# Kernel optimization log

Hardware: AMD Instinct MI355X
Metric: run time of the kernel (lower is better)

The kernel has to match this reference:

```python
import jax, jax.numpy as jnp
import numpy as np

D_MODEL = 1024
N_HEADS = 16
D_K = D_MODEL // N_HEADS
LN_EPS = 1e-5
NEG = -1e9


def setup_inputs() -> dict:
    key = jax.random.key(0)
    ks = jax.random.split(key, 12)
    B, S = 4, 2048
    s = 1.0 / np.sqrt(D_MODEL)
    # causal mask (1 = keep, 0 = masked)
    causal = jnp.tril(jnp.ones((S, S), dtype=jnp.int32))
    mask = jnp.broadcast_to(causal[None, None], (B, 1, S, S))
    return {
        "Q": jax.random.normal(ks[0], (B, S, D_MODEL), jnp.float32),
        "K": jax.random.normal(ks[1], (B, S, D_MODEL), jnp.float32),
        "V": jax.random.normal(ks[2], (B, S, D_MODEL), jnp.float32),
        "mask": mask,
        "Wq": jax.random.normal(ks[3], (D_MODEL, D_MODEL), jnp.float32) * s,
        "bq": jnp.zeros((D_MODEL,), jnp.float32),
        "Wk": jax.random.normal(ks[4], (D_MODEL, D_MODEL), jnp.float32) * s,
        "bk": jnp.zeros((D_MODEL,), jnp.float32),
        "Wv": jax.random.normal(ks[5], (D_MODEL, D_MODEL), jnp.float32) * s,
        "bv": jnp.zeros((D_MODEL,), jnp.float32),
        "Wo": jax.random.normal(ks[6], (D_MODEL, D_MODEL), jnp.float32) * s,
        "bo": jnp.zeros((D_MODEL,), jnp.float32),
        "ln_gamma": jnp.ones((D_MODEL,), jnp.float32),
        "ln_beta": jnp.zeros((D_MODEL,), jnp.float32),
    }


def _split_heads(x, B, S):
    # (B,S,D) -> (B,H,S,d_k)
    return x.reshape(B, S, N_HEADS, D_K).transpose(0, 2, 1, 3)


def reference(Q, K, V, mask, Wq, bq, Wk, bk, Wv, bv, Wo, bo, ln_gamma, ln_beta):
    B, S, _ = Q.shape
    residual = Q
    q = _split_heads(Q @ Wq + bq, B, S)
    k = _split_heads(K @ Wk + bk, B, S)
    v = _split_heads(V @ Wv + bv, B, S)
    scores = jnp.einsum("bhqd,bhkd->bhqk", q, k) / np.sqrt(D_K).astype(np.float32)
    scores = jnp.where(mask == 0, jnp.float32(NEG), scores)
    attn = jax.nn.softmax(scores, axis=-1)  # dropout p=0 -> identity
    ctx = jnp.einsum("bhqk,bhkd->bhqd", attn, v)
    ctx = ctx.transpose(0, 2, 1, 3).reshape(B, S, D_MODEL)
    out = ctx @ Wo + bo
    x = out + residual
    mu = jnp.mean(x, axis=-1, keepdims=True)
    var = jnp.mean(jnp.square(x - mu), axis=-1, keepdims=True)
    y = (x - mu) * jax.lax.rsqrt(var + LN_EPS) * ln_gamma + ln_beta
    return (y, attn)
```

## Files before the change

### kernel.cpp

```cpp
#include <hip/hip_runtime.h>

#define D_MODEL 1024
#define NH 16
#define DKH 64
#define SEQ 2048
#define BATCH 4
#define ROWS (BATCH*SEQ)

typedef _Float16 f16;
typedef _Float16 f16x4 __attribute__((ext_vector_type(4)));
typedef _Float16 f16x8 __attribute__((ext_vector_type(8)));
typedef float f32x4 __attribute__((ext_vector_type(4)));

#define MFMA16(a,b,c) __builtin_amdgcn_mfma_f32_16x16x32_f16((a),(b),(c),0,0,0)

__device__ __forceinline__ void gload16(const void* g, void* l) {
  __builtin_amdgcn_global_load_lds((const __attribute__((address_space(1))) void*)g,
                                   (__attribute__((address_space(3))) void*)l,
                                   16, 0, 0);
}


__global__ __launch_bounds__(256) void cvt_w_kernel(const float* __restrict__ Wq,
    const float* __restrict__ Wk, const float* __restrict__ Wv, const float* __restrict__ Wo,
    f16* __restrict__ dst)
{
  const float* W = (blockIdx.z==0)?Wq:(blockIdx.z==1)?Wk:(blockIdx.z==2)?Wv:Wo;
  f16* d = dst + (size_t)blockIdx.z * ((size_t)D_MODEL*D_MODEL);
  int idx = blockIdx.x*256 + threadIdx.x;
  int k = idx>>10, n = idx&1023;
  d[(size_t)n*D_MODEL + k] = (f16)W[idx];
}


template<int AF32>
__global__ __launch_bounds__(256) void gemm128(
    const void* __restrict__ A0, const void* __restrict__ A1, const void* __restrict__ A2,
    const f16* __restrict__ WTbase,
    const float* __restrict__ bias0, const float* __restrict__ bias1, const float* __restrict__ bias2,
    f16* __restrict__ out0, f16* __restrict__ out1, f16* __restrict__ out2,
    const float* __restrict__ resid, float* __restrict__ xout, int modeBase)
{
  __shared__ f16 Al[2][128*32];
  __shared__ f16 Bl[2][128*32];
  const int t = threadIdx.x, w = t>>6, l = t&63;
  const int nwg = (int)gridDim.x;
  const int wg = ((int)blockIdx.x & 7) * (nwg >> 3) + ((int)blockIdx.x >> 3);
  const int z  = wg >> 9;
  const int r2 = wg & 511;
  const int bm = r2 >> 3, bn = r2 & 7;
  const int mode = modeBase + z;
  const f16* WT = WTbase + (size_t)mode * ((size_t)D_MODEL*D_MODEL);
  const float* bias = (mode==0)?bias0:(mode==1)?bias1:(mode==2)?bias2:bias0;
  const int wm = w>>1, wn = w&1;
  const int lr = l>>2, lc = l&3, fr = l&15, fg = l>>4;
  f32x4 acc[4][4] = {};
  const char* Bb = (const char*)(WT + (size_t)bn*128*D_MODEL);

#define STAGEB(bufv, ktv) do { \
    char* Bd = (char*)&Bl[0][0] + (bufv)*8192; \
    _Pragma("unroll") \
    for (int cc=0; cc<2; ++cc) { \
      int r0 = w*32 + cc*16; \
      gload16(Bb + (size_t)(r0+lr)*2048 + (ktv)*64 + lc*16, Bd + r0*64); \
    } \
  } while(0)

#define COMPUTEK(bufv) do { \
    const f16* Ac = (const f16*)((char*)&Al[0][0] + (bufv)*8192); \
    const f16* Bc = (const f16*)((char*)&Bl[0][0] + (bufv)*8192); \
    f16x8 a[4], b[4]; \
    _Pragma("unroll") \
    for (int i=0;i<4;++i) a[i] = *(const f16x8*)(Ac + (wm*64+i*16+fr)*32 + fg*8); \
    _Pragma("unroll") \
    for (int j=0;j<4;++j) b[j] = *(const f16x8*)(Bc + (wn*64+j*16+fr)*32 + fg*8); \
    _Pragma("unroll") \
    for (int i=0;i<4;++i) \
      _Pragma("unroll") \
      for (int j=0;j<4;++j) \
        acc[i][j] = MFMA16(a[i], b[j], acc[i][j]); \
  } while(0)

  if constexpr (AF32) {
    const float* A32 = (const float*)((z==0)?A0:(z==1)?A1:A2);
    const float* Arow = A32 + (size_t)(bm*128 + w*32 + (l>>2))*1024 + (l&3)*8;
    f32x4 la[2][2];
    auto LOADA = [&](int ktv) {
      #pragma unroll
      for (int s=0;s<2;++s)
        #pragma unroll
        for (int q=0;q<2;++q)
          la[s][q] = *(const f32x4*)(Arow + (size_t)s*16*1024 + ktv*32 + q*4);
    };
    auto WRITEA = [&](int bufv) {
      char* Ad = (char*)&Al[0][0] + bufv*8192 + w*2048 + l*16;
      #pragma unroll
      for (int s=0;s<2;++s) {
        f16x8 pk;
        #pragma unroll
        for (int q=0;q<2;++q)
          #pragma unroll
          for (int m=0;m<4;++m) pk[q*4+m] = (f16)la[s][q][m];
        *(f16x8*)(Ad + s*1024) = pk;
      }
    };
    LOADA(0); STAGEB(0, 0); WRITEA(0);
    __syncthreads();
    for (int kt=0; kt<31; ++kt) {
      const int cur = kt & 1;
      LOADA(kt+1);
      STAGEB(cur^1, kt+1);
      COMPUTEK(cur);
      WRITEA(cur^1);
      __syncthreads();
    }
    COMPUTEK(1);
  } else {
    const char* Ab = (const char*)((const f16*)A0 + (size_t)bm*128*D_MODEL);
    auto STAGEA = [&](int bufv, int ktv) {
      char* Ad = (char*)&Al[0][0] + bufv*8192;
      #pragma unroll
      for (int cc=0; cc<2; ++cc) {
        int r0 = w*32 + cc*16;
        gload16(Ab + (size_t)(r0+lr)*2048 + ktv*64 + lc*16, Ad + r0*64);
      }
    };
    STAGEA(0,0); STAGEB(0, 0);
    asm volatile("s_waitcnt vmcnt(0)" ::: "memory");
    __builtin_amdgcn_s_barrier();
    for (int kt=0; kt<31; ++kt) {
      const int cur = kt & 1;
      STAGEA(cur^1, kt+1);
      STAGEB(cur^1, kt+1);
      COMPUTEK(cur);
      asm volatile("s_waitcnt vmcnt(0)" ::: "memory");
      __builtin_amdgcn_s_barrier();
    }
    COMPUTEK(1);
  }

#undef STAGEB
#undef COMPUTEK

  #pragma unroll
  for (int j=0;j<4;++j) {
    int col = bn*128 + wn*64 + j*16 + fr;
    float bz = bias[col];
    #pragma unroll
    for (int i=0;i<4;++i) {
      int row0 = bm*128 + wm*64 + i*16 + fg*4;
      f32x4 v = acc[i][j];
      if (mode==0) {
        int hh = col>>6, dk = col&63;
        #pragma unroll
        for (int r=0;r<4;++r) {
          int row = row0+r; int b_ = row>>11, s = row&(SEQ-1);
          out0[((size_t)(b_*NH+hh)*SEQ + s)*DKH + dk] = (f16)((v[r]+bz)*0.125f);
        }
      } else if (mode==1) {
        int hh = col>>6, dk = col&63;
        #pragma unroll
        for (int r=0;r<4;++r) {
          int row = row0+r; int b_ = row>>11, s = row&(SEQ-1);
          out1[((size_t)(b_*NH+hh)*SEQ + s)*DKH + dk] = (f16)(v[r]+bz);
        }
      } else if (mode==2) {
        int hh = col>>6, dk = col&63;
        int b_ = row0>>11, s0 = row0&(SEQ-1);
        f16x4 pk;
        #pragma unroll
        for (int r=0;r<4;++r) pk[r] = (f16)(v[r]+bz);
        *(f16x4*)(out2 + ((size_t)(b_*NH+hh)*DKH + dk)*SEQ + s0) = pk;
      } else {
        #pragma unroll
        for (int r=0;r<4;++r) {
          size_t o = (size_t)(row0+r)*D_MODEL + col;
          xout[o] = v[r] + bz + resid[o];
        }
      }
    }
  }
}


__global__ __launch_bounds__(256) void attn_kernel(
    const f16* __restrict__ qws, const f16* __restrict__ kws, const f16* __restrict__ vTws,
    float* __restrict__ attn, f16* __restrict__ ctx)
{
  __shared__ f16 el[4][32*128];
  const int t = threadIdx.x, w = t>>6, l = t&63;
  const int wg = ((int)blockIdx.x & 7)*64 + ((int)blockIdx.x >> 3);
  const int bh = wg >> 3;
  const int pr = wg & 7;
  const int qtA = pr, qtB = 15 - pr;
  const int fr = l & 15, fg = l >> 4;
  const f16* kp = kws + (size_t)bh*SEQ*DKH;
  const f16* vp = vTws + (size_t)bh*DKH*SEQ;
  const f16* qpA = qws + ((size_t)bh*SEQ + (size_t)qtA*128)*DKH;
  const f16* qpB = qws + ((size_t)bh*SEQ + (size_t)qtB*128)*DKH;
  float* apA = attn + ((size_t)bh*SEQ + (size_t)qtA*128)*SEQ;
  float* apB = attn + ((size_t)bh*SEQ + (size_t)qtB*128)*SEQ;
  f16* elw = (f16*)&el[w][0];
  const int swzx = (fr & 7) << 2;
  const int rbrow = l >> 5;
  const int rbslot = l & 31;

  f16x8 qfA[2][2], qfB[2][2];
  #pragma unroll
  for (int i=0;i<2;++i)
    #pragma unroll
    for (int kc=0;kc<2;++kc) {
      qfA[i][kc] = *(const f16x8*)(qpA + (w*32 + i*16 + fr)*DKH + kc*32 + fg*8);
      qfB[i][kc] = *(const f16x8*)(qpB + (w*32 + i*16 + fr)*DKH + kc*32 + fg*8);
    }

  auto fill_tile = [&](float* apr, int kt2) {
    f32x4 z4 = {0.f,0.f,0.f,0.f};
    #pragma unroll
    for (int i2=0;i2<16;++i2) {
      int idx = t + i2*256;
      int row = idx >> 5, c4 = idx & 31;
      __builtin_nontemporal_store(z4, (f32x4*)(apr + (size_t)row*SEQ + (size_t)kt2*128 + c4*4));
    }
  };
  const int cB = pr;

  float psumA[2] = {0.f,0.f}, psumB[2] = {0.f,0.f};
  int u = 0, f = 0;
  const int np1 = qtB + 1;
  auto drip_fills = [&]() {
    while (f*np1 < u*15) {
      if (f < cB) fill_tile(apB, qtB+1+f);
      else        fill_tile(apA, qtA+1+(f-cB));
      ++f;
    }
  };

  for (int kt=0; kt<=qtA; ++kt) {
    const f16* kb = kp + (size_t)kt*128*DKH;
    const bool diagA = (kt == qtA);
    #pragma unroll
    for (int jh=0; jh<2; ++jh) {
      f32x4 scB[2][4] = {};
      f32x4 scA[2][4] = {};
      #pragma unroll
      for (int j2=0;j2<4;++j2) {
        const int j = jh*4 + j2;
        #pragma unroll
        for (int kc=0;kc<2;++kc) {
          f16x8 kf = *(const f16x8*)(kb + (j*16+fr)*DKH + kc*32 + fg*8);
          scB[0][j2] = MFMA16(kf, qfB[0][kc], scB[0][j2]);
          scB[1][j2] = MFMA16(kf, qfB[1][kc], scB[1][j2]);
          scA[0][j2] = MFMA16(kf, qfA[0][kc], scA[0][j2]);
          scA[1][j2] = MFMA16(kf, qfA[1][kc], scA[1][j2]);
        }
      }
      #pragma unroll
      for (int i=0;i<2;++i)
        #pragma unroll
        for (int j2=0;j2<4;++j2)
          #pragma unroll
          for (int r=0;r<4;++r) psumB[i] += __expf(scB[i][j2][r]);
      if (diagA) {
        #pragma unroll
        for (int i=0;i<2;++i) {
          int rloc = w*32 + i*16 + fr;
          #pragma unroll
          for (int j2=0;j2<4;++j2)
            #pragma unroll
            for (int r=0;r<4;++r) {
              int cloc = (jh*4+j2)*16 + fg*4 + r;
              if (cloc <= rloc) psumA[i] += __expf(scA[i][j2][r]);
            }
        }
      } else {
        #pragma unroll
        for (int i=0;i<2;++i)
          #pragma unroll
          for (int j2=0;j2<4;++j2)
            #pragma unroll
            for (int r=0;r<4;++r) psumA[i] += __expf(scA[i][j2][r]);
      }
    }
    ++u; drip_fills();
  }

  for (int kt=qtA+1; kt<=qtB; ++kt) {
    const f16* kb = kp + (size_t)kt*128*DKH;
    const bool diagB = (kt == qtB);
    #pragma unroll
    for (int jh=0; jh<2; ++jh) {
      f32x4 sc[2][4] = {};
      #pragma unroll
      for (int j2=0;j2<4;++j2) {
        const int j = jh*4 + j2;
        #pragma unroll
        for (int kc=0;kc<2;++kc) {
          f16x8 kf = *(const f16x8*)(kb + (j*16+fr)*DKH + kc*32 + fg*8);
          sc[0][j2] = MFMA16(kf, qfB[0][kc], sc[0][j2]);
          sc[1][j2] = MFMA16(kf, qfB[1][kc], sc[1][j2]);
        }
      }
      if (diagB) {
        #pragma unroll
        for (int i=0;i<2;++i) {
          int rloc = w*32 + i*16 + fr;
          #pragma unroll
          for (int j2=0;j2<4;++j2)
            #pragma unroll
            for (int r=0;r<4;++r) {
              int cloc = (jh*4+j2)*16 + fg*4 + r;
              if (cloc <= rloc) psumB[i] += __expf(sc[i][j2][r]);
            }
        }
      } else {
        #pragma unroll
        for (int i=0;i<2;++i)
          #pragma unroll
          for (int j2=0;j2<4;++j2)
            #pragma unroll
            for (int r=0;r<4;++r) psumB[i] += __expf(sc[i][j2][r]);
      }
    }
    ++u; drip_fills();
  }

  #pragma unroll
  for (int m=16; m<64; m<<=1) {
    psumA[0] += __shfl_xor(psumA[0], m, 64);
    psumA[1] += __shfl_xor(psumA[1], m, 64);
    psumB[0] += __shfl_xor(psumB[0], m, 64);
    psumB[1] += __shfl_xor(psumB[1], m, 64);
  }
  float rinvA[2] = {1.f/psumA[0], 1.f/psumA[1]};
  float rinvB[2] = {1.f/psumB[0], 1.f/psumB[1]};

  f32x4 av[2][4];
  auto pass2_tile = [&](int ktv, bool diag, const f16x8 (&qf)[2][2], const float (&rinv)[2], float* apr) {
    const f16* kb = kp + (size_t)ktv*128*DKH;
    #pragma unroll
    for (int jh=0; jh<2; ++jh) {
      f32x4 sc[2][4] = {};
      __builtin_amdgcn_s_setprio(1);
      #pragma unroll
      for (int j2=0;j2<4;++j2) {
        const int j = jh*4 + j2;
        #pragma unroll
        for (int kc=0;kc<2;++kc) {
          f16x8 kf = *(const f16x8*)(kb + (j*16+fr)*DKH + kc*32 + fg*8);
          sc[0][j2] = MFMA16(kf, qf[0][kc], sc[0][j2]);
          sc[1][j2] = MFMA16(kf, qf[1][kc], sc[1][j2]);
        }
      }
      __builtin_amdgcn_s_setprio(0);
      #pragma unroll
      for (int i=0;i<2;++i) {
        const int rloc = w*32 + i*16 + fr;
        #pragma unroll
        for (int j2=0;j2<4;++j2) {
          const int j = jh*4 + j2;
          f16x4 ef;
          #pragma unroll
          for (int r=0;r<4;++r) {
            int cloc = j*16 + fg*4 + r;
            float e = (diag && cloc > rloc) ? 0.f : __expf(sc[i][j2][r]) * rinv[i];
            ef[r] = (f16)e;
          }
          *(f16x4*)(elw + (i*16+fr)*128 + (((j*4+fg) ^ swzx) << 2)) = ef;
        }
      }
    }
    {
      float* apk = apr + (size_t)(w*32)*SEQ + (size_t)ktv*128;
      #pragma unroll
      for (int p=0;p<16;++p) {
        int row = p*2 + rbrow;
        f16x4 pv4 = *(const f16x4*)(elw + row*128 + ((rbslot ^ ((row&7)<<2)) << 2));
        f32x4 o4; o4[0]=(float)pv4[0]; o4[1]=(float)pv4[1]; o4[2]=(float)pv4[2]; o4[3]=(float)pv4[3];
        __builtin_nontemporal_store(o4, (f32x4*)(apk + (size_t)row*SEQ + rbslot*4));
      }
    }
    __builtin_amdgcn_s_setprio(1);
    #pragma unroll
    for (int c=0;c<4;++c) {
      f16x8 pf0 = *(const f16x8*)(elw + (fr)*128    + (((c*8+fg*2) ^ swzx) << 2));
      f16x8 pf1 = *(const f16x8*)(elw + (16+fr)*128 + (((c*8+fg*2) ^ swzx) << 2));
      #pragma unroll
      for (int j2=0;j2<4;++j2) {
        f16x8 vf = *(const f16x8*)(vp + (j2*16+fr)*SEQ + ktv*128 + c*32 + fg*8);
        av[0][j2] = MFMA16(vf, pf0, av[0][j2]);
        av[1][j2] = MFMA16(vf, pf1, av[1][j2]);
      }
    }
    __builtin_amdgcn_s_setprio(0);
  };
  auto ctx_store = [&](int qtv) {
    const int b_ = bh >> 4, hh = bh & 15;
    #pragma unroll
    for (int i=0;i<2;++i) {
      size_t rowoff = ((size_t)b_*SEQ + (size_t)qtv*128 + w*32 + i*16 + fr) * D_MODEL + hh*DKH;
      #pragma unroll
      for (int j2=0;j2<4;++j2) {
        f16x4 pk;
        #pragma unroll
        for (int r=0;r<4;++r) pk[r] = (f16)av[i][j2][r];
        *(f16x4*)(ctx + rowoff + j2*16 + fg*4) = pk;
      }
    }
  };

  #pragma unroll
  for (int i=0;i<2;++i)
    #pragma unroll
    for (int j2=0;j2<4;++j2) av[i][j2] = (f32x4){0.f,0.f,0.f,0.f};
  for (int kt=0; kt<=qtA; ++kt) pass2_tile(kt, kt==qtA, qfA, rinvA, apA);
  ctx_store(qtA);

  #pragma unroll
  for (int i=0;i<2;++i)
    #pragma unroll
    for (int j2=0;j2<4;++j2) av[i][j2] = (f32x4){0.f,0.f,0.f,0.f};
  for (int kt=0; kt<=qtB; ++kt) pass2_tile(kt, kt==qtB, qfB, rinvB, apB);
  ctx_store(qtB);
}


__global__ __launch_bounds__(256) void ln_kernel(const float* __restrict__ x,
    const float* __restrict__ gamma, const float* __restrict__ beta, float* __restrict__ y)
{
  __shared__ float red[4];
  __shared__ float red2[4];
  const int t = threadIdx.x, w = t>>6, l = t&63;
  const size_t row = blockIdx.x;
  float4 v = ((const float4*)(x + row*D_MODEL))[t];
  float s = v.x+v.y+v.z+v.w;
  #pragma unroll
  for (int m=1;m<64;m<<=1) s += __shfl_xor(s, m, 64);
  if (l==0) red[w] = s;
  __syncthreads();
  float mu = (red[0]+red[1]+red[2]+red[3]) * (1.f/D_MODEL);
  float dx=v.x-mu, dy=v.y-mu, dz=v.z-mu, dw=v.w-mu;
  float q = dx*dx+dy*dy+dz*dz+dw*dw;
  #pragma unroll
  for (int m=1;m<64;m<<=1) q += __shfl_xor(q, m, 64);
  if (l==0) red2[w] = q;
  __syncthreads();
  float var = (red2[0]+red2[1]+red2[2]+red2[3]) * (1.f/D_MODEL);
  float rs = rsqrtf(var + 1e-5f);
  float4 g  = ((const float4*)gamma)[t];
  float4 bb = ((const float4*)beta)[t];
  float4 o;
  o.x = dx*rs*g.x + bb.x;
  o.y = dy*rs*g.y + bb.y;
  o.z = dz*rs*g.z + bb.z;
  o.w = dw*rs*g.w + bb.w;
  ((float4*)(y + row*D_MODEL))[t] = o;
}


extern "C" void kernel_launch(void* const* d_in, const int* in_sizes, int n_in,
                              void* d_out, int out_size, void* d_ws, size_t ws_size,
                              hipStream_t stream)
{
  const float* Q  = (const float*)d_in[0];
  const float* K  = (const float*)d_in[1];
  const float* V  = (const float*)d_in[2];
  const float* Wq = (const float*)d_in[4];
  const float* bq = (const float*)d_in[5];
  const float* Wk = (const float*)d_in[6];
  const float* bk = (const float*)d_in[7];
  const float* Wv = (const float*)d_in[8];
  const float* bv = (const float*)d_in[9];
  const float* Wo = (const float*)d_in[10];
  const float* bo = (const float*)d_in[11];
  const float* gam= (const float*)d_in[12];
  const float* bet= (const float*)d_in[13];

  float* y    = (float*)d_out;
  float* attn = y + (size_t)ROWS*D_MODEL;

  char* ws = (char*)d_ws;
  const size_t SZ = (size_t)ROWS*D_MODEL*sizeof(f16);
  f16* ctx   = (f16*)ws;
  float* xb  = (float*)(ws + SZ);
  f16* WT    = (f16*)(ws + 3*SZ);
  f16* qws   = (f16*)(ws + 3*SZ + ((size_t)4*D_MODEL*D_MODEL*sizeof(f16)));
  f16* kws   = (f16*)((char*)qws + SZ);
  f16* vT    = (f16*)((char*)kws + SZ);

  cvt_w_kernel<<<dim3(4096,1,4), 256, 0, stream>>>(Wq, Wk, Wv, Wo, WT);
  gemm128<1><<<1536, 256, 0, stream>>>(Q, K, V, WT, bq, bk, bv, qws, kws, vT, nullptr, nullptr, 0);
  attn_kernel<<<512, 256, 0, stream>>>(qws, kws, vT, attn, ctx);
  gemm128<0><<<512, 256, 0, stream>>>(ctx, nullptr, nullptr, WT, bo, bo, bo, nullptr, nullptr, nullptr, Q, xb, 3);
  ln_kernel<<<8192, 256, 0, stream>>>(xb, gam, bet, y);
}
```

Measured before the change: 476.3 us.

## Deepen GEMM K-loop pipelining with partial vmcnt waits and register double-buffering

```diff
diff --git a/kernel.cpp b/kernel.cpp
--- a/kernel.cpp
+++ b/kernel.cpp
@@ -13,6 +13,7 @@
 typedef float f32x4 __attribute__((ext_vector_type(4)));
 
 #define MFMA16(a,b,c) __builtin_amdgcn_mfma_f32_16x16x32_f16((a),(b),(c),0,0,0)
+#define CFENCE() asm volatile("" ::: "memory")
 
 __device__ __forceinline__ void gload16(const void* g, void* l) {
   __builtin_amdgcn_global_load_lds((const __attribute__((address_space(1))) void*)g,
@@ -81,39 +82,65 @@
         acc[i][j] = MFMA16(a[i], b[j], acc[i][j]); \
   } while(0)
 
+#define LOADA_TO(dst, ktv) do { \
+    _Pragma("unroll") \
+    for (int s=0;s<2;++s) \
+      _Pragma("unroll") \
+      for (int q=0;q<2;++q) \
+        dst[s][q] = *(const f32x4*)(Arow + (size_t)s*16*1024 + (ktv)*32 + q*4); \
+  } while(0)
+
+#define WRITEA_FROM(src, bufv) do { \
+    char* Ad = (char*)&Al[0][0] + (bufv)*8192 + w*2048 + l*16; \
+    _Pragma("unroll") \
+    for (int s=0;s<2;++s) { \
+      f16x8 pk; \
+      _Pragma("unroll") \
+      for (int q=0;q<2;++q) \
+        _Pragma("unroll") \
+        for (int m2=0;m2<4;++m2) pk[q*4+m2] = (f16)src[s][q][m2]; \
+      *(f16x8*)(Ad + s*1024) = pk; \
+    } \
+  } while(0)
+
+#define BAR_FENCED() do { __builtin_amdgcn_s_barrier(); CFENCE(); } while(0)
+
   if constexpr (AF32) {
     const float* A32 = (const float*)((z==0)?A0:(z==1)?A1:A2);
     const float* Arow = A32 + (size_t)(bm*128 + w*32 + (l>>2))*1024 + (l&3)*8;
-    f32x4 la[2][2];
-    auto LOADA = [&](int ktv) {
-      #pragma unroll
-      for (int s=0;s<2;++s)
-        #pragma unroll
-        for (int q=0;q<2;++q)
-          la[s][q] = *(const f32x4*)(Arow + (size_t)s*16*1024 + ktv*32 + q*4);
-    };
-    auto WRITEA = [&](int bufv) {
-      char* Ad = (char*)&Al[0][0] + bufv*8192 + w*2048 + l*16;
-      #pragma unroll
-      for (int s=0;s<2;++s) {
-        f16x8 pk;
-        #pragma unroll
-        for (int q=0;q<2;++q)
-          #pragma unroll
-          for (int m=0;m<4;++m) pk[q*4+m] = (f16)la[s][q][m];
-        *(f16x8*)(Ad + s*1024) = pk;
-      }
-    };
-    LOADA(0); STAGEB(0, 0); WRITEA(0);
-    __syncthreads();
-    for (int kt=0; kt<31; ++kt) {
-      const int cur = kt & 1;
-      LOADA(kt+1);
-      STAGEB(cur^1, kt+1);
-      COMPUTEK(cur);
-      WRITEA(cur^1);
-      __syncthreads();
-    }
+    f32x4 laA[2][2], laB[2][2];
+    LOADA_TO(laA, 0);
+    STAGEB(0, 0);
+    WRITEA_FROM(laA, 0);
+    LOADA_TO(laB, 1);
+    CFENCE();
+    for (int kt2=0; kt2<30; kt2+=2) {
+      STAGEB((kt2+1)&1, kt2+1);
+      LOADA_TO(laA, kt2+2);
+      asm volatile("s_waitcnt vmcnt(6) lgkmcnt(0)" ::: "memory");
+      BAR_FENCED();
+      COMPUTEK(kt2&1);
+      WRITEA_FROM(laB, (kt2+1)&1);
+      CFENCE();
+      BAR_FENCED();
+      STAGEB((kt2+2)&1, kt2+2);
+      LOADA_TO(laB, kt2+3);
+      asm volatile("s_waitcnt vmcnt(6) lgkmcnt(0)" ::: "memory");
+      BAR_FENCED();
+      COMPUTEK((kt2+1)&1);
+      WRITEA_FROM(laA, (kt2+2)&1);
+      CFENCE();
+      BAR_FENCED();
+    }
+    STAGEB(1, 31);
+    asm volatile("s_waitcnt vmcnt(6) lgkmcnt(0)" ::: "memory");
+    BAR_FENCED();
+    COMPUTEK(0);
+    WRITEA_FROM(laB, 1);
+    CFENCE();
+    BAR_FENCED();
+    asm volatile("s_waitcnt vmcnt(0) lgkmcnt(0)" ::: "memory");
+    BAR_FENCED();
     COMPUTEK(1);
   } else {
     const char* Ab = (const char*)((const f16*)A0 + (size_t)bm*128*D_MODEL);
@@ -126,21 +153,27 @@
       }
     };
     STAGEA(0,0); STAGEB(0, 0);
-    asm volatile("s_waitcnt vmcnt(0)" ::: "memory");
-    __builtin_amdgcn_s_barrier();
+    CFENCE();
     for (int kt=0; kt<31; ++kt) {
       const int cur = kt & 1;
       STAGEA(cur^1, kt+1);
       STAGEB(cur^1, kt+1);
+      asm volatile("s_waitcnt vmcnt(4)" ::: "memory");
+      BAR_FENCED();
       COMPUTEK(cur);
-      asm volatile("s_waitcnt vmcnt(0)" ::: "memory");
-      __builtin_amdgcn_s_barrier();
-    }
+      CFENCE();
+      BAR_FENCED();
+    }
+    asm volatile("s_waitcnt vmcnt(0)" ::: "memory");
+    BAR_FENCED();
     COMPUTEK(1);
   }
 
 #undef STAGEB
 #undef COMPUTEK
+#undef LOADA_TO
+#undef WRITEA_FROM
+#undef BAR_FENCED
 
   #pragma unroll
   for (int j=0;j<4;++j) {
```

Measured after the change: 465.6 us. 1.02x faster.
